# Performance work log

Hardware: AMD Instinct MI355X
Metric: run time of the kernel (lower is better)

## Reference

```python
import jax, jax.numpy as jnp
import numpy as np
import math

SQRT32 = math.sqrt(32.0)


def _l2norm(x, eps=1e-12):
    # matches torch.nn.functional.normalize(dim=-1): x / max(||x||, eps)
    n = jnp.linalg.norm(x, axis=-1, keepdims=True)
    return x / jnp.maximum(n, eps)


def setup_inputs() -> dict:
    key = jax.random.key(0)
    k1, k2 = jax.random.split(key)
    z = jax.random.normal(k1, (8, 256, 32, 32), dtype=jnp.float32)
    # trunc_normal_(std=0.02) init approximated by scaled normal
    embed_weight = jax.random.normal(k2, (16384, 256), dtype=jnp.float32) * 0.02
    return {"z": z, "embed_weight": embed_weight}


def reference(z, embed_weight):
    # z: [b, d, h, w] channel-first -> pack to [b*h*w, d]
    b, d, h, w = z.shape
    zf = jnp.transpose(z, (0, 2, 3, 1)).reshape(-1, d)  # [N, d]

    # l2_norm=True, no predefined codebook: distance = -z @ normalize(E)^T
    ew = _l2norm(embed_weight)                          # [K, d]
    dist = -(zf @ ew.T)                                 # [N, K]
    min_encoding_indices = jnp.argmin(dist, axis=1)     # [N]

    # gather UNnormalized embedding rows, then normalize (as in source)
    z_q = _l2norm(embed_weight[min_encoding_indices])   # [N, d]

    # straight-through estimator
    z_q = zf + jax.lax.stop_gradient(z_q - zf)

    loss = jnp.zeros((1,), dtype=z.dtype)

    # unpack to [b, h, w, d]
    zq_bhwd = z_q.reshape(b, h, w, d)
    # torch .long() truncates toward zero; astype(int) does the same
    bit_indices = (zq_bhwd * SQRT32).astype(jnp.int32) + 4
    zq_out = jnp.transpose(zq_bhwd, (0, 3, 1, 2))       # [b, d, h, w]

    return zq_out, min_encoding_indices, bit_indices, loss
```

## Files before the change

### kernel.cpp

```cpp
#include <hip/hip_runtime.h>
#include <math.h>

#define D      256
#define K      16384
#define NPTS   8192
#define DELTA  0.2f
#define LCAP   1024
#define MAXCAP 4000000u

#define O_IDX  2097152
#define O_BIT  2105344
#define O_LOSS 4202496

typedef __attribute__((ext_vector_type(8))) short bf16x8;
typedef __attribute__((ext_vector_type(4))) float f32x4;
typedef unsigned long long u64;

__device__ __forceinline__ unsigned f2s(float f) {
    unsigned u = __float_as_uint(f);
    return (u & 0x80000000u) ? ~u : (u | 0x80000000u);
}
__device__ __forceinline__ float s2f(unsigned s) {
    return __uint_as_float((s & 0x80000000u) ? (s & 0x7fffffffu) : ~s);
}
__device__ __forceinline__ unsigned short f2bf(float f) {
    unsigned u = __float_as_uint(f);
    u += 0x7fffu + ((u >> 16) & 1u);
    return (unsigned short)(u >> 16);
}
__device__ __forceinline__ void gl2lds16(const unsigned short* g, unsigned short* l) {
    __builtin_amdgcn_global_load_lds(
        (const __attribute__((address_space(1))) void*)g,
        (__attribute__((address_space(3))) void*)l, 16, 0, 0);
}

__global__ __launch_bounds__(256) void prep(const float* __restrict__ E,
                                            const float* __restrict__ z,
                                            float* __restrict__ den,
                                            unsigned short* __restrict__ ewb,
                                            unsigned short* __restrict__ zfb,
                                            float* __restrict__ zf32,
                                            unsigned* __restrict__ gmax,
                                            u64* __restrict__ keys,
                                            unsigned* __restrict__ cnt) {
    const int blk = blockIdx.x, tid = threadIdx.x;
    if (blk < 512) {
        const int lane = tid & 63, wave = tid >> 6;
        if (blk < 32)        gmax[blk * 256 + tid] = 0u;
        else if (blk < 64)   keys[(blk - 32) * 256 + tid] = 0ull;
        else if (blk == 64 && tid < 2) cnt[tid] = 0u;
        #pragma unroll
        for (int j = 0; j < 8; ++j) {
            const int row = blk * 32 + wave * 8 + j;
            const float4 v = *(const float4*)(E + (size_t)row * D + lane * 4);
            float ss = v.x * v.x + v.y * v.y + v.z * v.z + v.w * v.w;
            #pragma unroll
            for (int o = 1; o < 64; o <<= 1) ss += __shfl_xor(ss, o);
            const float dn = fmaxf(sqrtf(ss), 1e-12f);
            const unsigned lo = (unsigned)f2bf(v.x / dn) | ((unsigned)f2bf(v.y / dn) << 16);
            const unsigned hi = (unsigned)f2bf(v.z / dn) | ((unsigned)f2bf(v.w / dn) << 16);
            *(uint2*)(ewb + (size_t)row * D + lane * 4) = make_uint2(lo, hi);
            if (lane == 0) den[row] = dn;
        }
    } else {
        const int bi = blk - 512;
        const int b = bi >> 4, hw0 = (bi & 15) * 64;
        __shared__ float t[64][65];
        for (int dc = 0; dc < D; dc += 64) {
            #pragma unroll
            for (int it = 0; it < 16; ++it) {
                const int idx = it * 256 + tid;
                const int dl = idx >> 6, hw = idx & 63;
                t[dl][hw] = z[(size_t)(b * 256 + dc + dl) * 1024 + hw0 + hw];
            }
            __syncthreads();
            #pragma unroll
            for (int it = 0; it < 16; ++it) {
                const int idx = it * 256 + tid;
                const int pl = idx >> 6, dl = idx & 63;
                const float v = t[dl][pl];
                const size_t o = (size_t)(b * 1024 + hw0 + pl) * D + dc + dl;
                zfb[o]  = f2bf(v);
                zf32[o] = v;
            }
            __syncthreads();
        }
    }
}

#define GEMM_CORE()                                                                 \
    f32x4 acc[4][4];                                                                \
    _Pragma("unroll")                                                               \
    for (int i = 0; i < 4; ++i)                                                     \
        _Pragma("unroll")                                                           \
        for (int j = 0; j < 4; ++j) acc[i][j] = (f32x4){0.f, 0.f, 0.f, 0.f};        \
    {                                                                               \
        const int srow = lane >> 2, schk = (lane & 3) * 8;                          \
        const unsigned short* gA = zfb + (size_t)(m0 + wave * 32 + srow) * D + schk;\
        const unsigned short* gB = ewb + (size_t)(n0 + wave * 32 + srow) * D + schk;\
        unsigned short* lA = &za[(wave * 32) * 32];                                 \
        unsigned short* lB = &eb[(wave * 32) * 32];                                 \
        for (int dc = 0; dc < D; dc += 32) {                                        \
            __syncthreads();                                                        \
            gl2lds16(gA + dc,          lA);                                         \
            gl2lds16(gA + dc + 16 * D, lA + 16 * 32);                               \
            gl2lds16(gB + dc,          lB);                                         \
            gl2lds16(gB + dc + 16 * D, lB + 16 * 32);                               \
            __syncthreads();                                                        \
            bf16x8 af[4], bfr[4];                                                   \
            _Pragma("unroll")                                                       \
            for (int mt = 0; mt < 4; ++mt)                                          \
                af[mt] = *(const bf16x8*)&za[(wm * 64 + mt * 16 + col) * 32 + quad * 8]; \
            _Pragma("unroll")                                                       \
            for (int nt = 0; nt < 4; ++nt)                                          \
                bfr[nt] = *(const bf16x8*)&eb[(wn * 64 + nt * 16 + col) * 32 + quad * 8]; \
            _Pragma("unroll")                                                       \
            for (int mt = 0; mt < 4; ++mt)                                          \
                _Pragma("unroll")                                                   \
                for (int nt = 0; nt < 4; ++nt)                                      \
                    acc[mt][nt] = __builtin_amdgcn_mfma_f32_16x16x32_bf16(af[mt], bfr[nt], \
                                                                          acc[mt][nt], 0, 0, 0); \
        }                                                                           \
    }

__global__ __launch_bounds__(256, 3) void score_seed(const unsigned short* __restrict__ zfb,
                                                     const unsigned short* __restrict__ ewb,
                                                     unsigned* __restrict__ gmax,
                                                     u64* __restrict__ cand,
                                                     unsigned* __restrict__ cnt,
                                                     unsigned cap) {
    __shared__ __align__(16) unsigned short za[128 * 32];
    __shared__ __align__(16) unsigned short eb[128 * 32];
    __shared__ unsigned thrS[128];
    __shared__ u64 lbuf[LCAP];
    __shared__ unsigned lcount, lbase;

    const int tid = threadIdx.x, lane = tid & 63, wave = tid >> 6;
    const int quad = lane >> 4, col = lane & 15;
    const int wm = wave >> 1, wn = wave & 1;
    const int m0 = blockIdx.x * 128;
    const int n0 = blockIdx.y * 128;
    const int shsrc = lane & 48;

    if (tid < 128) thrS[tid] = 0u;
    if (tid == 0) lcount = 0u;

    GEMM_CORE()

    float red[4][4];
    #pragma unroll
    for (int mt = 0; mt < 4; ++mt)
        #pragma unroll
        for (int r = 0; r < 4; ++r)
            red[mt][r] = fmaxf(fmaxf(acc[mt][0][r], acc[mt][1][r]),
                               fmaxf(acc[mt][2][r], acc[mt][3][r]));
    #pragma unroll
    for (int off = 1; off < 16; off <<= 1)
        #pragma unroll
        for (int mt = 0; mt < 4; ++mt)
            #pragma unroll
            for (int r = 0; r < 4; ++r)
                red[mt][r] = fmaxf(red[mt][r], __shfl_xor(red[mt][r], off));
    #pragma unroll
    for (int mt = 0; mt < 4; ++mt)
        #pragma unroll
        for (int r = 0; r < 4; ++r) {
            const int pl = wm * 64 + mt * 16 + quad * 4 + r;
            unsigned cur = 0;
            if (col == 0) {
                const unsigned enc = f2s(red[mt][r]);
                const unsigned old = atomicMax(&thrS[pl], enc);
                cur = old > enc ? old : enc;
            }
            cur = (unsigned)__shfl((int)cur, shsrc);
            red[mt][r] = s2f(cur) - DELTA;
        }

    const int ncode0 = n0 + wn * 64 + col;
    #pragma unroll
    for (int mt = 0; mt < 4; ++mt) {
        #pragma unroll
        for (int r = 0; r < 4; ++r) {
            const float tp = red[mt][r];
            const unsigned pt = m0 + wm * 64 + mt * 16 + quad * 4 + r;
            #pragma unroll
            for (int nt = 0; nt < 4; ++nt) {
                const float v = acc[mt][nt][r];
                if (v >= tp) {
                    const unsigned slot = atomicAdd(&lcount, 1u);
                    const u64 e = ((u64)((pt << 14) | (unsigned)(ncode0 + nt * 16)) << 32)
                                  | f2s(v);
                    if (slot < LCAP) lbuf[slot] = e;
                    else {
                        const unsigned g = atomicAdd(cnt, 1u);
                        if (g < cap) cand[g] = e;
                    }
                }
            }
        }
    }

    __syncthreads();
    if (tid < 128) atomicMax(&gmax[m0 + tid], thrS[tid]);
    const unsigned m_ = lcount < LCAP ? lcount : LCAP;
    if (tid == 0) lbase = atomicAdd(cnt, m_);
    __syncthreads();
    for (unsigned i = tid; i < m_; i += 256) {
        const unsigned g = lbase + i;
        if (g < cap) cand[g] = lbuf[i];
    }
}

__global__ __launch_bounds__(256, 3) void score_main(const unsigned short* __restrict__ zfb,
                                                     const unsigned short* __restrict__ ewb,
                                                     const unsigned* __restrict__ gmax,
                                                     u64* __restrict__ cand,
                                                     unsigned* __restrict__ cnt,
                                                     unsigned cap) {
    __shared__ __align__(16) unsigned short za[128 * 32];
    __shared__ __align__(16) unsigned short eb[128 * 32];
    __shared__ float thrL[128];
    __shared__ u64 lbuf[LCAP];
    __shared__ unsigned lcount, lbase;

    const int tid = threadIdx.x, lane = tid & 63, wave = tid >> 6;
    const int quad = lane >> 4, col = lane & 15;
    const int wm = wave >> 1, wn = wave & 1;
    const int m0 = blockIdx.x * 128;
    const int n0 = (16 + blockIdx.y) * 128;

    if (tid < 128) thrL[tid] = s2f(gmax[m0 + tid]) - DELTA;
    if (tid == 0) lcount = 0u;

    GEMM_CORE()

    const int ncode0 = n0 + wn * 64 + col;
    #pragma unroll
    for (int mt = 0; mt < 4; ++mt) {
        #pragma unroll
        for (int r = 0; r < 4; ++r) {
            const int pl = wm * 64 + mt * 16 + quad * 4 + r;
            const float tp = thrL[pl];
            #pragma unroll
            for (int nt = 0; nt < 4; ++nt) {
                const float v = acc[mt][nt][r];
                if (v >= tp) {
                    const unsigned slot = atomicAdd(&lcount, 1u);
                    const u64 e = ((u64)(((unsigned)pl + m0) << 14 | (unsigned)(ncode0 + nt * 16)) << 32)
                                  | f2s(v);
                    if (slot < LCAP) lbuf[slot] = e;
                    else {
                        const unsigned g = atomicAdd(cnt, 1u);
                        if (g < cap) cand[g] = e;
                    }
                }
            }
        }
    }

    __syncthreads();
    const unsigned m_ = lcount < LCAP ? lcount : LCAP;
    if (tid == 0) lbase = atomicAdd(cnt, m_);
    __syncthreads();
    for (unsigned i = tid; i < m_; i += 256) {
        const unsigned g = lbase + i;
        if (g < cap) cand[g] = lbuf[i];
    }
}

__global__ __launch_bounds__(256) void cand_max(const u64* __restrict__ cand,
                                                const unsigned* __restrict__ cnt,
                                                unsigned* __restrict__ gmax,
                                                unsigned cap) {
    const unsigned total = min(cnt[0], cap);
    const unsigned stride = gridDim.x * 256;
    for (unsigned i = blockIdx.x * 256 + threadIdx.x; i < total; i += stride) {
        const u64 e = cand[i];
        atomicMax(&gmax[(unsigned)(e >> 46)], (unsigned)(e & 0xffffffffull));
    }
}

__global__ __launch_bounds__(256) void rescore(const float* __restrict__ zf32,
                                               const float* __restrict__ E,
                                               const float* __restrict__ den,
                                               const unsigned* __restrict__ gmax,
                                               const u64* __restrict__ cand,
                                               const unsigned* __restrict__ cnt,
                                               u64* __restrict__ keys,
                                               unsigned cap) {
    const unsigned total = min(cnt[0], cap);
    const int lane = threadIdx.x & 63;
    const unsigned w = (blockIdx.x * 256 + threadIdx.x) >> 6;
    const unsigned nw = gridDim.x * 4;
    for (unsigned base = w * 64; base < total; base += nw * 64) {
        const unsigned i = base + lane;
        u64 e = 0;
        bool keep = false;
        if (i < total) {
            e = cand[i];
            const int p = (int)(e >> 46);
            keep = (s2f((unsigned)(e & 0xffffffffull)) >= s2f(gmax[p]) - DELTA);
        }
        u64 mask = __ballot(keep);
        while (mask) {
            const int src = __ffsll((long long)mask) - 1;
            mask &= mask - 1;
            const unsigned pc = (unsigned)__shfl((int)(unsigned)(e >> 32), src);
            const int p = pc >> 14, c = pc & 16383;
            const float dinv = 1.0f / den[c];
            const float4 a = *(const float4*)(zf32 + (size_t)p * D + lane * 4);
            const float4 b = *(const float4*)(E + (size_t)c * D + lane * 4);
            float sv = fmaf(a.x, b.x * dinv, fmaf(a.y, b.y * dinv,
                       fmaf(a.z, b.z * dinv, a.w * (b.w * dinv))));
            #pragma unroll
            for (int o = 1; o < 64; o <<= 1) sv += __shfl_xor(sv, o);
            if (lane == 0)
                atomicMax(keys + p, ((u64)f2s(sv) << 32) | (unsigned)(16383 - c));
        }
    }
}

__global__ __launch_bounds__(256) void finalize(const float* __restrict__ E,
                                                const float* __restrict__ den,
                                                const u64* __restrict__ keys,
                                                float* __restrict__ out) {
    __shared__ float t[32][257];
    __shared__ int sIdx[32];
    __shared__ float sDen[32];
    const int tid = threadIdx.x;
    const int n0 = blockIdx.x * 32;
    if (tid < 32) {
        const u64 key = keys[n0 + tid];
        const int idx = 16383 - (int)(unsigned)(key & 0xffffffffull);
        sIdx[tid] = idx;
        sDen[tid] = den[idx];
        out[O_IDX + n0 + tid] = (float)idx;
    }
    __syncthreads();
    const float S = 5.65685424949238019520675489683895f;
    #pragma unroll 4
    for (int i = 0; i < 32; ++i) {
        const float v = E[(size_t)sIdx[i] * D + tid] / sDen[i];
        t[i][tid] = v;
        out[O_BIT + (size_t)(n0 + i) * D + tid] = (float)((int)(v * S) + 4);
    }
    __syncthreads();
    const int b = n0 >> 10, hw0 = n0 & 1023;
    const int hwl = tid & 31, cg = tid >> 5;
    #pragma unroll 4
    for (int cc = 0; cc < 32; ++cc) {
        const int c = cc * 8 + cg;
        out[(size_t)(b * 256 + c) * 1024 + hw0 + hwl] = t[hwl][c];
    }
    if (n0 == 0 && tid == 0) out[O_LOSS] = 0.0f;
}

extern "C" void kernel_launch(void* const* d_in, const int* in_sizes, int n_in,
                              void* d_out, int out_size, void* d_ws, size_t ws_size,
                              hipStream_t stream) {
    const float* z = (const float*)d_in[0];
    const float* E = (const float*)d_in[1];
    float* out = (float*)d_out;

    char* w = (char*)d_ws;
    unsigned short* ewb  = (unsigned short*)w;  w += (size_t)K * D * 2;
    unsigned short* zfb  = (unsigned short*)w;  w += (size_t)NPTS * D * 2;
    float*          zf32 = (float*)w;           w += (size_t)NPTS * D * 4;
    u64*            keys = (u64*)w;             w += (size_t)NPTS * 8;
    float*          den  = (float*)w;           w += (size_t)K * 4;
    unsigned*       gmax = (unsigned*)w;        w += (size_t)NPTS * 4;
    unsigned*       cnt  = (unsigned*)w;        w += 256;
    u64*            cand = (u64*)w;
    const size_t fixed = (size_t)(w - (char*)d_ws);
    const size_t avail = ws_size > fixed ? (ws_size - fixed) / 8 : 0;
    const unsigned cap = (unsigned)(avail < (size_t)MAXCAP ? avail : (size_t)MAXCAP);

    prep<<<640, 256, 0, stream>>>(E, z, den, ewb, zfb, zf32, gmax, keys, cnt);

    dim3 gpre(NPTS / 128, 16);
    score_seed<<<gpre, 256, 0, stream>>>(zfb, ewb, gmax, cand, cnt, cap);
    dim3 gmain(NPTS / 128, 112);
    score_main<<<gmain, 256, 0, stream>>>(zfb, ewb, gmax, cand, cnt, cap);

    cand_max<<<256, 256, 0, stream>>>(cand, cnt, gmax, cap);
    rescore<<<1024, 256, 0, stream>>>(zf32, E, den, gmax, cand, cnt, keys, cap);
    finalize<<<NPTS / 32, 256, 0, stream>>>(E, den, keys, out);
}
```

Baseline: 280.5 us.

## Load GEMM fragments directly from global via k-blocked transposed bf16 layout

The prep kernel now writes the normalized codebook and the bf16 points in a k-chunk-major layout (8 bf16 per chunk, rows contiguous), so each lane's MFMA fragment is one contiguous 16-byte global load. The GEMM core drops the LDS staging, the global_load_lds copies and the per-step barriers, and reads fragments straight from global/L2. This removes LDS traffic and synchronisation, but gives up on-chip reuse across waves: each wave reloads operands that other waves in the block share, so it leans on L2 bandwidth and latency hiding, with no double buffering.

```diff
diff --git a/kernel.cpp b/kernel.cpp
--- a/kernel.cpp
+++ b/kernel.cpp
@@ -28,17 +28,13 @@
     u += 0x7fffu + ((u >> 16) & 1u);
     return (unsigned short)(u >> 16);
 }
-__device__ __forceinline__ void gl2lds16(const unsigned short* g, unsigned short* l) {
-    __builtin_amdgcn_global_load_lds(
-        (const __attribute__((address_space(1))) void*)g,
-        (__attribute__((address_space(3))) void*)l, 16, 0, 0);
-}
+
 
 __global__ __launch_bounds__(256) void prep(const float* __restrict__ E,
                                             const float* __restrict__ z,
                                             float* __restrict__ den,
-                                            unsigned short* __restrict__ ewb,
-                                            unsigned short* __restrict__ zfb,
+                                            unsigned short* __restrict__ ewbT,
+                                            unsigned short* __restrict__ zfbT,
                                             float* __restrict__ zf32,
                                             unsigned* __restrict__ gmax,
                                             u64* __restrict__ keys,
@@ -59,7 +55,8 @@
             const float dn = fmaxf(sqrtf(ss), 1e-12f);
             const unsigned lo = (unsigned)f2bf(v.x / dn) | ((unsigned)f2bf(v.y / dn) << 16);
             const unsigned hi = (unsigned)f2bf(v.z / dn) | ((unsigned)f2bf(v.w / dn) << 16);
-            *(uint2*)(ewb + (size_t)row * D + lane * 4) = make_uint2(lo, hi);
+            *(uint2*)(ewbT + ((size_t)(lane >> 1) * K + row) * 8 + (lane & 1) * 4)
+                = make_uint2(lo, hi);
             if (lane == 0) den[row] = dn;
         }
     } else {
@@ -79,9 +76,9 @@
                 const int idx = it * 256 + tid;
                 const int pl = idx >> 6, dl = idx & 63;
                 const float v = t[dl][pl];
-                const size_t o = (size_t)(b * 1024 + hw0 + pl) * D + dc + dl;
-                zfb[o]  = f2bf(v);
-                zf32[o] = v;
+                const int p = b * 1024 + hw0 + pl, k = dc + dl;
+                zfbT[((size_t)(k >> 3) * NPTS + p) * 8 + (k & 7)] = f2bf(v);
+                zf32[(size_t)p * D + k] = v;
             }
             __syncthreads();
         }
@@ -95,25 +92,17 @@
         _Pragma("unroll")                                                           \
         for (int j = 0; j < 4; ++j) acc[i][j] = (f32x4){0.f, 0.f, 0.f, 0.f};        \
     {                                                                               \
-        const int srow = lane >> 2, schk = (lane & 3) * 8;                          \
-        const unsigned short* gA = zfb + (size_t)(m0 + wave * 32 + srow) * D + schk;\
-        const unsigned short* gB = ewb + (size_t)(n0 + wave * 32 + srow) * D + schk;\
-        unsigned short* lA = &za[(wave * 32) * 32];                                 \
-        unsigned short* lB = &eb[(wave * 32) * 32];                                 \
-        for (int dc = 0; dc < D; dc += 32) {                                        \
-            __syncthreads();                                                        \
-            gl2lds16(gA + dc,          lA);                                         \
-            gl2lds16(gA + dc + 16 * D, lA + 16 * 32);                               \
-            gl2lds16(gB + dc,          lB);                                         \
-            gl2lds16(gB + dc + 16 * D, lB + 16 * 32);                               \
-            __syncthreads();                                                        \
+        const unsigned short* pA = zfbT + ((size_t)quad * NPTS + m0 + wm * 64 + col) * 8; \
+        const unsigned short* pB = ewbT + ((size_t)quad * K    + n0 + wn * 64 + col) * 8; \
+        _Pragma("unroll")                                                           \
+        for (int dc = 0; dc < 8; ++dc) {                                            \
             bf16x8 af[4], bfr[4];                                                   \
             _Pragma("unroll")                                                       \
             for (int mt = 0; mt < 4; ++mt)                                          \
-                af[mt] = *(const bf16x8*)&za[(wm * 64 + mt * 16 + col) * 32 + quad * 8]; \
+                af[mt] = *(const bf16x8*)(pA + (size_t)dc * 4 * NPTS * 8 + mt * 128);\
             _Pragma("unroll")                                                       \
             for (int nt = 0; nt < 4; ++nt)                                          \
-                bfr[nt] = *(const bf16x8*)&eb[(wn * 64 + nt * 16 + col) * 32 + quad * 8]; \
+                bfr[nt] = *(const bf16x8*)(pB + (size_t)dc * 4 * K * 8 + nt * 128); \
             _Pragma("unroll")                                                       \
             for (int mt = 0; mt < 4; ++mt)                                          \
                 _Pragma("unroll")                                                   \
@@ -123,14 +112,12 @@
         }                                                                           \
     }
 
-__global__ __launch_bounds__(256, 3) void score_seed(const unsigned short* __restrict__ zfb,
-                                                     const unsigned short* __restrict__ ewb,
+__global__ __launch_bounds__(256, 3) void score_seed(const unsigned short* __restrict__ zfbT,
+                                                     const unsigned short* __restrict__ ewbT,
                                                      unsigned* __restrict__ gmax,
                                                      u64* __restrict__ cand,
                                                      unsigned* __restrict__ cnt,
                                                      unsigned cap) {
-    __shared__ __align__(16) unsigned short za[128 * 32];
-    __shared__ __align__(16) unsigned short eb[128 * 32];
     __shared__ unsigned thrS[128];
     __shared__ u64 lbuf[LCAP];
     __shared__ unsigned lcount, lbase;
@@ -146,6 +133,7 @@
     if (tid == 0) lcount = 0u;
 
     GEMM_CORE()
+    __syncthreads();
 
     float red[4][4];
     #pragma unroll
@@ -211,14 +199,12 @@
     }
 }
 
-__global__ __launch_bounds__(256, 3) void score_main(const unsigned short* __restrict__ zfb,
-                                                     const unsigned short* __restrict__ ewb,
+__global__ __launch_bounds__(256, 3) void score_main(const unsigned short* __restrict__ zfbT,
+                                                     const unsigned short* __restrict__ ewbT,
                                                      const unsigned* __restrict__ gmax,
                                                      u64* __restrict__ cand,
                                                      unsigned* __restrict__ cnt,
                                                      unsigned cap) {
-    __shared__ __align__(16) unsigned short za[128 * 32];
-    __shared__ __align__(16) unsigned short eb[128 * 32];
     __shared__ float thrL[128];
     __shared__ u64 lbuf[LCAP];
     __shared__ unsigned lcount, lbase;
@@ -233,6 +219,7 @@
     if (tid == 0) lcount = 0u;
 
     GEMM_CORE()
+    __syncthreads();
 
     const int ncode0 = n0 + wn * 64 + col;
     #pragma unroll
@@ -363,8 +350,8 @@
     float* out = (float*)d_out;
 
     char* w = (char*)d_ws;
-    unsigned short* ewb  = (unsigned short*)w;  w += (size_t)K * D * 2;
-    unsigned short* zfb  = (unsigned short*)w;  w += (size_t)NPTS * D * 2;
+    unsigned short* ewbT = (unsigned short*)w;  w += (size_t)K * D * 2;
+    unsigned short* zfbT = (unsigned short*)w;  w += (size_t)NPTS * D * 2;
     float*          zf32 = (float*)w;           w += (size_t)NPTS * D * 4;
     u64*            keys = (u64*)w;             w += (size_t)NPTS * 8;
     float*          den  = (float*)w;           w += (size_t)K * 4;
@@ -375,12 +362,12 @@
     const size_t avail = ws_size > fixed ? (ws_size - fixed) / 8 : 0;
     const unsigned cap = (unsigned)(avail < (size_t)MAXCAP ? avail : (size_t)MAXCAP);
 
-    prep<<<640, 256, 0, stream>>>(E, z, den, ewb, zfb, zf32, gmax, keys, cnt);
+    prep<<<640, 256, 0, stream>>>(E, z, den, ewbT, zfbT, zf32, gmax, keys, cnt);
 
     dim3 gpre(NPTS / 128, 16);
-    score_seed<<<gpre, 256, 0, stream>>>(zfb, ewb, gmax, cand, cnt, cap);
+    score_seed<<<gpre, 256, 0, stream>>>(zfbT, ewbT, gmax, cand, cnt, cap);
     dim3 gmain(NPTS / 128, 112);
-    score_main<<<gmain, 256, 0, stream>>>(zfb, ewb, gmax, cand, cnt, cap);
+    score_main<<<gmain, 256, 0, stream>>>(zfbT, ewbT, gmax, cand, cnt, cap);
 
     cand_max<<<256, 256, 0, stream>>>(cand, cnt, gmax, cap);
     rescore<<<1024, 256, 0, stream>>>(zf32, E, den, gmax, cand, cnt, keys, cap);
```

New measurement: 265.6 us. 1.06x faster.
